# Kernel optimization log

Measured on AMD Instinct MI355X. Metric: run time of the kernel, lower is better.

## Reference

```python
import jax, jax.numpy as jnp
import numpy as np

B, S, D, EXP = 2, 2048, 128, 16
N = D * EXP  # state_dim = 2048


def setup_inputs() -> dict:
    key = jax.random.key(0)
    ks = jax.random.split(key, 11)
    s_in = 1.0 / np.sqrt(D)   # torch Linear default init bound for dim->N layers
    s_out = 1.0 / np.sqrt(N)  # for out_proj (N->dim)
    x = jax.random.normal(ks[0], (B, S, D), dtype=jnp.float32)
    W_B = jax.random.uniform(ks[1], (N, D), jnp.float32, -s_in, s_in)
    b_B = jax.random.uniform(ks[2], (N,), jnp.float32, -s_in, s_in)
    W_C = jax.random.uniform(ks[3], (N, D), jnp.float32, -s_in, s_in)
    b_C = jax.random.uniform(ks[4], (N,), jnp.float32, -s_in, s_in)
    W_dt = jax.random.uniform(ks[5], (N, D), jnp.float32, -s_in, s_in)
    b_dt = jax.random.uniform(ks[6], (N,), jnp.float32, -s_in, s_in)
    A_log = jnp.log(jax.random.uniform(ks[7], (N,), jnp.float32) * 0.5 + 0.5)
    W_out = jax.random.uniform(ks[8], (D, N), jnp.float32, -s_out, s_out)
    b_out = jax.random.uniform(ks[9], (D,), jnp.float32, -s_out, s_out)
    return {"x": x, "W_B": W_B, "b_B": b_B, "W_C": W_C, "b_C": b_C,
            "W_dt": W_dt, "b_dt": b_dt, "A_log": A_log,
            "W_out": W_out, "b_out": b_out}


def reference(x, W_B, b_B, W_C, b_C, W_dt, b_dt, A_log, W_out, b_out):
    # Featurizer projections: [B,S,D] -> [B,S,N]
    B_feat = jnp.einsum('bsd,nd->bsn', x, W_B) + b_B
    C_feat = jnp.einsum('bsd,nd->bsn', x, W_C) + b_C
    dt = jax.nn.softplus(jnp.einsum('bsd,nd->bsn', x, W_dt) + b_dt)
    A = -jnp.exp(A_log)                # [N]
    A_bar = jnp.exp(dt * A)            # [B,S,N]
    B_bar = dt * B_feat                # [B,S,N]

    # Sequential diagonal scan: h_t = A_t * h_{t-1} + B_t ; y_t = C_t * h_t
    def step(h, abc):
        a_t, b_t, c_t = abc            # each [B,N]
        h = a_t * h + b_t
        return h, c_t * h

    h0 = jnp.zeros((x.shape[0], N), dtype=x.dtype)
    xs = (jnp.swapaxes(A_bar, 0, 1),   # [S,B,N]
          jnp.swapaxes(B_bar, 0, 1),
          jnp.swapaxes(C_feat, 0, 1))
    _, ys = jax.lax.scan(step, h0, xs)  # ys: [S,B,N]
    y = jnp.swapaxes(ys, 0, 1)          # [B,S,N]
    return jnp.einsum('bsn,dn->bsd', y, W_out) + b_out
```

## Files before the change

### kernel.cpp

```cpp
#include <hip/hip_runtime.h>


#define BB 2
#define SS 2048
#define DDIM 128
#define NDIM 2048
#define TT (BB*SS)
#define NTILE (TT/16)

typedef short short8 __attribute__((ext_vector_type(8)));
typedef float floatx4 __attribute__((ext_vector_type(4)));

__device__ __forceinline__ unsigned short f2b(float f){
  unsigned u = __float_as_uint(f);
  u += 0x7FFFu + ((u >> 16) & 1u);
  return (unsigned short)(u >> 16);
}
__device__ __forceinline__ float softplus_f(float v){
  return v > 15.f ? v : __logf(1.f + __expf(v));
}
__device__ __forceinline__ void pack8(const float* __restrict__ s,
                                      unsigned short* __restrict__ d){
  floatx4 v0 = *(const floatx4*)s;
  floatx4 v1 = *(const floatx4*)(s + 4);
  short8 r;
  r[0]=(short)f2b(v0[0]); r[1]=(short)f2b(v0[1]); r[2]=(short)f2b(v0[2]); r[3]=(short)f2b(v0[3]);
  r[4]=(short)f2b(v1[0]); r[5]=(short)f2b(v1[1]); r[6]=(short)f2b(v1[2]); r[7]=(short)f2b(v1[3]);
  *(short8*)d = r;
}

__global__ void prep_kernel(const float* __restrict__ x,
                            const float* __restrict__ W_B,
                            const float* __restrict__ W_C,
                            const float* __restrict__ W_dt,
                            const float* __restrict__ A_log,
                            const float* __restrict__ W_out,
                            unsigned short* __restrict__ xp,
                            unsigned short* __restrict__ Wp3,
                            unsigned short* __restrict__ Wop,
                            float* __restrict__ Aval,
                            unsigned long long* __restrict__ Sbuf){
  const int gid = blockIdx.x * blockDim.x + threadIdx.x;
  if (gid < 32768) Sbuf[gid] = 0ull;
  if (gid < 2048) Aval[gid] = -__expf(A_log[gid]);
  if (gid < 65536){
    int g = gid, tile = g >> 8, kk = (g >> 6) & 3, lane = g & 63;
    int q = lane >> 4, m = lane & 15;
    pack8(x + (size_t)(tile*16 + m)*DDIM + kk*32 + q*8, xp + (size_t)g*8);
  }
  if (gid < 98304){
    int mat = gid >> 15, g = gid & 32767;
    const float* W = (mat == 0) ? W_B : (mat == 1 ? W_dt : W_C);
    int tile = g >> 8, kk = (g >> 6) & 3, lane = g & 63;
    int q = lane >> 4, m = lane & 15;
    pack8(W + (size_t)(tile*16 + m)*DDIM + kk*32 + q*8,
          Wp3 + (size_t)mat*262144 + (size_t)g*8);
  }
  if (gid < 32768){
    int g = gid, tile = g >> 12, kk = (g >> 6) & 63, lane = g & 63;
    int q = lane >> 4, m = lane & 15;
    pack8(W_out + (size_t)(tile*16 + m)*NDIM + kk*32 + q*8, Wop + (size_t)g*8);
  }
}

__global__ __launch_bounds__(256, 2) void projscan_kernel(
    const unsigned short* __restrict__ xp,
    const unsigned short* __restrict__ Wp3,
    const float* __restrict__ b_B,
    const float* __restrict__ b_dt,
    const float* __restrict__ b_C,
    const float* __restrict__ Aval,
    unsigned long long* __restrict__ Sbuf,
    unsigned short* __restrict__ ybp){
  __shared__ unsigned short sW[3*4096];
  __shared__ unsigned short sYT[4][16*40];
  __shared__ float sPw[4][32], sHw[4][32];
  __shared__ float sIw[4][32];
  const int tid  = threadIdx.x;
  const int lane = tid & 63;
  const int wv   = tid >> 6;
  const int m    = lane & 15;
  const int q    = lane >> 4;
  const int p    = blockIdx.y * 16 + blockIdx.x;
  const int xcd  = p & 7;
  const int slot = p >> 3;
  const int rr   = slot & 15;
  const int j    = slot >> 4;
  const int row  = xcd*16 + rr;
  const int by   = row >> 1;
  const int bx   = (row & 1)*8 + j;
  const int n0   = by*32;

  for (int i = tid; i < 1536; i += 256){
    int mat = i >> 9, rem = i & 511;
    *(short8*)(sW + mat*4096 + rem*8) =
        *(const short8*)(Wp3 + (size_t)mat*262144 + (size_t)by*4096 + rem*8);
  }
  __syncthreads();

  float bBv[2], bDv[2], bCv[2], Avv[2];
#pragma unroll
  for (int nt = 0; nt < 2; ++nt){
    const int n = n0 + nt*16 + m;
    bBv[nt] = b_B[n]; bDv[nt] = b_dt[n]; bCv[nt] = b_C[n]; Avv[nt] = Aval[n];
  }

  unsigned ypk[4][2][2], cpk[4][2][2];
  float pe_t[4][2], he_t[4][2];
  float pa_run[2] = {1.f, 1.f}, ha_run[2] = {0.f, 0.f};

#pragma unroll
  for (int i = 0; i < 4; ++i){
    const int tile = bx*16 + wv*4 + i;
    short8 xf[4];
#pragma unroll
    for (int kk = 0; kk < 4; ++kk)
      xf[kk] = *(const short8*)(xp + (size_t)tile*2048 + kk*512 + lane*8);

    floatx4 acc[3][2];
#pragma unroll
    for (int mat = 0; mat < 3; ++mat)
#pragma unroll
      for (int nt = 0; nt < 2; ++nt)
        acc[mat][nt] = (floatx4){0.f,0.f,0.f,0.f};
#pragma unroll
    for (int nt = 0; nt < 2; ++nt)
#pragma unroll
      for (int kk = 0; kk < 4; ++kk){
        short8 wB = *(const short8*)(sW +         nt*2048 + kk*512 + lane*8);
        short8 wD = *(const short8*)(sW + 4096 +  nt*2048 + kk*512 + lane*8);
        short8 wC = *(const short8*)(sW + 8192 +  nt*2048 + kk*512 + lane*8);
        acc[0][nt] = __builtin_amdgcn_mfma_f32_16x16x32_bf16(xf[kk], wB, acc[0][nt], 0, 0, 0);
        acc[1][nt] = __builtin_amdgcn_mfma_f32_16x16x32_bf16(xf[kk], wD, acc[1][nt], 0, 0, 0);
        acc[2][nt] = __builtin_amdgcn_mfma_f32_16x16x32_bf16(xf[kk], wC, acc[2][nt], 0, 0, 0);
      }

#pragma unroll
    for (int nt = 0; nt < 2; ++nt){
      float Ar[4], Br[4], Cc[4];
#pragma unroll
      for (int r = 0; r < 4; ++r){
        float dtv = softplus_f(acc[1][nt][r] + bDv[nt]);
        Ar[r] = __expf(dtv * Avv[nt]);
        Br[r] = dtv * (acc[0][nt][r] + bBv[nt]);
        Cc[r] = acc[2][nt][r] + bCv[nt];
      }
      float P = Ar[0], H = Br[0];
#pragma unroll
      for (int r = 1; r < 4; ++r){ H = Ar[r]*H + Br[r]; P *= Ar[r]; }
      float pp = __shfl(P, (lane - 16) & 63, 64);
      float hh = __shfl(H, (lane - 16) & 63, 64);
      if (q >= 1){ H = P*hh + H; P *= pp; }
      pp = __shfl(P, (lane - 32) & 63, 64);
      hh = __shfl(H, (lane - 32) & 63, 64);
      if (q >= 2){ H = P*hh + H; P *= pp; }
      float pe = __shfl(P, (lane - 16) & 63, 64);
      float he = __shfl(H, (lane - 16) & 63, 64);
      if (q == 0){ pe = 1.f; he = 0.f; }
      float pb = __shfl(P, m + 48, 64);
      float hb = __shfl(H, m + 48, 64);

      float h = he, pa = pe;
      unsigned short yr[4], cr[4];
#pragma unroll
      for (int r = 0; r < 4; ++r){
        h = Ar[r]*h + Br[r];
        pa *= Ar[r];
        yr[r] = f2b(Cc[r]*h);
        cr[r] = f2b(Cc[r]*pa);
      }
      ypk[i][nt][0] = (unsigned)yr[0] | ((unsigned)yr[1] << 16);
      ypk[i][nt][1] = (unsigned)yr[2] | ((unsigned)yr[3] << 16);
      cpk[i][nt][0] = (unsigned)cr[0] | ((unsigned)cr[1] << 16);
      cpk[i][nt][1] = (unsigned)cr[2] | ((unsigned)cr[3] << 16);

      pe_t[i][nt] = pa_run[nt];
      he_t[i][nt] = ha_run[nt];
      ha_run[nt] = pb*ha_run[nt] + hb;
      pa_run[nt] *= pb;
    }
  }
  if (q == 0){
#pragma unroll
    for (int nt = 0; nt < 2; ++nt){
      sPw[wv][nt*16 + m] = pa_run[nt];
      sHw[wv][nt*16 + m] = ha_run[nt];
    }
  }
  __syncthreads();

  if (tid < 32){
    float Pw[4], Hw[4];
#pragma unroll
    for (int w2 = 0; w2 < 4; ++w2){ Pw[w2] = sPw[w2][tid]; Hw[w2] = sHw[w2][tid]; }
    float pb = 1.f, hb = 0.f;
#pragma unroll
    for (int w2 = 0; w2 < 4; ++w2){ hb = Pw[w2]*hb + Hw[w2]; pb *= Pw[w2]; }
    float pbc = fmaxf(pb, 1e-30f);
    __hip_atomic_store(Sbuf + (size_t)(by*16 + bx)*32 + tid,
        ((unsigned long long)__float_as_uint(pbc) << 32) |
         (unsigned long long)__float_as_uint(hb),
        __ATOMIC_RELAXED, __HIP_MEMORY_SCOPE_AGENT);
    float S = 0.f;
    const int cnt = bx & 7;
    if (cnt){
      const int j0 = bx & ~7;
      unsigned long long v0=0,v1=0,v2=0,v3=0,v4=0,v5=0,v6=0;
      unsigned got = 0;
      const unsigned all = (1u << cnt) - 1u;
      const unsigned long long* base = Sbuf + (size_t)(by*16 + j0)*32 + tid;
      for (;;){
#define LOOKBACK(J, V)                                                          \
        if (J < cnt && !(got & (1u << J))){                                     \
          unsigned long long a = __hip_atomic_load(base + (size_t)J*32,         \
              __ATOMIC_RELAXED, __HIP_MEMORY_SCOPE_AGENT);                      \
          if ((unsigned)(a >> 32) != 0u){ V = a; got |= 1u << J; }              \
        }
        LOOKBACK(0, v0) LOOKBACK(1, v1) LOOKBACK(2, v2) LOOKBACK(3, v3)
        LOOKBACK(4, v4) LOOKBACK(5, v5) LOOKBACK(6, v6)
#undef LOOKBACK
        if (got == all) break;
        __builtin_amdgcn_s_sleep(1);
      }
#define COMPOSE(J, V)                                                           \
      if (J < cnt) S = __uint_as_float((unsigned)(V >> 32))*S +                 \
                       __uint_as_float((unsigned)V);
      COMPOSE(0, v0) COMPOSE(1, v1) COMPOSE(2, v2) COMPOSE(3, v3)
      COMPOSE(4, v4) COMPOSE(5, v5) COMPOSE(6, v6)
#undef COMPOSE
    }
    float s = S;
#pragma unroll
    for (int w2 = 0; w2 < 4; ++w2){
      sIw[w2][tid] = s;
      s = Pw[w2]*s + Hw[w2];
    }
  }
  __syncthreads();

  float iw[2];
#pragma unroll
  for (int nt = 0; nt < 2; ++nt) iw[nt] = sIw[wv][nt*16 + m];
#pragma unroll
  for (int i = 0; i < 4; ++i){
    const int tile = bx*16 + wv*4 + i;
#pragma unroll
    for (int nt = 0; nt < 2; ++nt){
      float it = pe_t[i][nt]*iw[nt] + he_t[i][nt];
#pragma unroll
      for (int j2 = 0; j2 < 2; ++j2){
        unsigned yp = ypk[i][nt][j2], cp = cpk[i][nt][j2];
        float y0 = __uint_as_float(yp << 16);
        float y1 = __uint_as_float(yp & 0xffff0000u);
        float c0 = __uint_as_float(cp << 16);
        float c1 = __uint_as_float(cp & 0xffff0000u);
        sYT[wv][(q*4 + j2*2 + 0)*40 + nt*16 + m] = f2b(y0 + c0*it);
        sYT[wv][(q*4 + j2*2 + 1)*40 + nt*16 + m] = f2b(y1 + c1*it);
      }
    }
    short8 yv = *(const short8*)&sYT[wv][m*40 + q*8];
    *(short8*)(ybp + (size_t)tile*32768 + (size_t)by*512 + (size_t)lane*8) = yv;
  }
}

__global__ void outproj_kernel(const unsigned short* __restrict__ ybp,
                               const unsigned short* __restrict__ Wop,
                               const float* __restrict__ b_out,
                               float* __restrict__ out){
  __shared__ float red[4*2048];
  const int tid  = threadIdx.x;
  const int lane = tid & 63;
  const int wv   = tid >> 6;
  const int m    = lane & 15;
  const int q    = lane >> 4;
  const int tile = blockIdx.x;

  floatx4 acc[8];
#pragma unroll
  for (int dt = 0; dt < 8; ++dt) acc[dt] = (floatx4){0.f,0.f,0.f,0.f};

  const unsigned short* aP = ybp + (size_t)tile*32768 + lane*8;
  const unsigned short* bP = Wop + (size_t)lane*8;
#pragma unroll 4
  for (int kk = wv*16; kk < wv*16 + 16; ++kk){
    short8 af = *(const short8*)(aP + (size_t)kk*512);
#pragma unroll
    for (int dt = 0; dt < 8; ++dt){
      short8 bf = *(const short8*)(bP + (size_t)dt*32768 + (size_t)kk*512);
      acc[dt] = __builtin_amdgcn_mfma_f32_16x16x32_bf16(af, bf, acc[dt], 0, 0, 0);
    }
  }
#pragma unroll
  for (int dt = 0; dt < 8; ++dt)
#pragma unroll
    for (int r = 0; r < 4; ++r)
      red[wv*2048 + (q*4 + r)*128 + dt*16 + m] = acc[dt][r];
  __syncthreads();
#pragma unroll
  for (int i = 0; i < 8; ++i){
    int idx = i*256 + tid;
    float s = red[idx] + red[2048 + idx] + red[4096 + idx] + red[6144 + idx];
    int tl = idx >> 7, d = idx & 127;
    out[(size_t)(tile*16 + tl)*DDIM + d] = s + b_out[d];
  }
}

extern "C" void kernel_launch(void* const* d_in, const int* in_sizes, int n_in,
                              void* d_out, int out_size, void* d_ws, size_t ws_size,
                              hipStream_t stream) {
  const float* x     = (const float*)d_in[0];
  const float* W_B   = (const float*)d_in[1];
  const float* b_B   = (const float*)d_in[2];
  const float* W_C   = (const float*)d_in[3];
  const float* b_C   = (const float*)d_in[4];
  const float* W_dt  = (const float*)d_in[5];
  const float* b_dt  = (const float*)d_in[6];
  const float* A_log = (const float*)d_in[7];
  const float* W_out = (const float*)d_in[8];
  const float* b_out = (const float*)d_in[9];
  float* out = (float*)d_out;

  char* w = (char*)d_ws;
  unsigned short* xp    = (unsigned short*)(w + 0x0000000);
  unsigned short* Wp3   = (unsigned short*)(w + 0x0100000);
  unsigned short* Wop   = (unsigned short*)(w + 0x0280000);
  float*          Aval  = (float*)         (w + 0x0300000);
  unsigned short* ybp   = (unsigned short*)(w + 0x0310000);
  unsigned long long* Sbuf = (unsigned long long*)(w + 0x1310000);

  prep_kernel<<<384, 256, 0, stream>>>(
      x, W_B, W_C, W_dt, A_log, W_out, xp, Wp3, Wop, Aval, Sbuf);

  projscan_kernel<<<dim3(16, 64), 256, 0, stream>>>(
      xp, Wp3, b_B, b_dt, b_C, Aval, Sbuf, ybp);

  outproj_kernel<<<NTILE, 256, 0, stream>>>(ybp, Wop, b_out, out);
}
```

Measured before the change: 115.5 us.

## Prefetch next x tile, use packed bf16 convert, alias LDS, back off lookback spin

The projection-scan kernel now double-buffers the x fragments, loading the next tile's inputs while the current tile's MFMAs run. Manual bf16 rounding and packing is replaced by the hardware v_cvt_pk_bf16_f32 instruction. The per-wave transpose buffer now reuses the weight LDS region after the MFMAs finish, which lowers LDS use, and the lookback spin uses an escalating sleep. Risks are higher register pressure from the double buffer, possible rounding differences from the hardware convert, and a race if any wave still reads sW when another wave writes sYT, since no barrier separates the two.

After: 115.3 us, median of 2. Within noise of the previous version (-0.2%).

```diff
diff --git a/kernel.cpp b/kernel.cpp
--- a/kernel.cpp
+++ b/kernel.cpp
@@ -15,6 +15,11 @@
   unsigned u = __float_as_uint(f);
   u += 0x7FFFu + ((u >> 16) & 1u);
   return (unsigned short)(u >> 16);
+}
+__device__ __forceinline__ unsigned cvt_pk_bf16(float lo, float hi){
+  unsigned r;
+  asm("v_cvt_pk_bf16_f32 %0, %1, %2" : "=v"(r) : "v"(lo), "v"(hi));
+  return r;
 }
 __device__ __forceinline__ float softplus_f(float v){
   return v > 15.f ? v : __logf(1.f + __expf(v));
@@ -73,7 +78,6 @@
     unsigned long long* __restrict__ Sbuf,
     unsigned short* __restrict__ ybp){
   __shared__ unsigned short sW[3*4096];
-  __shared__ unsigned short sYT[4][16*40];
   __shared__ float sPw[4][32], sHw[4][32];
   __shared__ float sIw[4][32];
   const int tid  = threadIdx.x;
@@ -90,6 +94,7 @@
   const int by   = row >> 1;
   const int bx   = (row & 1)*8 + j;
   const int n0   = by*32;
+  unsigned short* sYT = sW + wv*640;
 
   for (int i = tid; i < 1536; i += 256){
     int mat = i >> 9, rem = i & 511;
@@ -109,14 +114,17 @@
   float pe_t[4][2], he_t[4][2];
   float pa_run[2] = {1.f, 1.f}, ha_run[2] = {0.f, 0.f};
 
+  short8 xf[2][4];
+  {
+    const int t0 = bx*16 + wv*4;
+#pragma unroll
+    for (int kk = 0; kk < 4; ++kk)
+      xf[0][kk] = *(const short8*)(xp + (size_t)t0*2048 + kk*512 + lane*8);
+  }
+
 #pragma unroll
   for (int i = 0; i < 4; ++i){
-    const int tile = bx*16 + wv*4 + i;
-    short8 xf[4];
-#pragma unroll
-    for (int kk = 0; kk < 4; ++kk)
-      xf[kk] = *(const short8*)(xp + (size_t)tile*2048 + kk*512 + lane*8);
-
+    const int cur = i & 1;
     floatx4 acc[3][2];
 #pragma unroll
     for (int mat = 0; mat < 3; ++mat)
@@ -130,10 +138,16 @@
         short8 wB = *(const short8*)(sW +         nt*2048 + kk*512 + lane*8);
         short8 wD = *(const short8*)(sW + 4096 +  nt*2048 + kk*512 + lane*8);
         short8 wC = *(const short8*)(sW + 8192 +  nt*2048 + kk*512 + lane*8);
-        acc[0][nt] = __builtin_amdgcn_mfma_f32_16x16x32_bf16(xf[kk], wB, acc[0][nt], 0, 0, 0);
-        acc[1][nt] = __builtin_amdgcn_mfma_f32_16x16x32_bf16(xf[kk], wD, acc[1][nt], 0, 0, 0);
-        acc[2][nt] = __builtin_amdgcn_mfma_f32_16x16x32_bf16(xf[kk], wC, acc[2][nt], 0, 0, 0);
-      }
+        acc[0][nt] = __builtin_amdgcn_mfma_f32_16x16x32_bf16(xf[cur][kk], wB, acc[0][nt], 0, 0, 0);
+        acc[1][nt] = __builtin_amdgcn_mfma_f32_16x16x32_bf16(xf[cur][kk], wD, acc[1][nt], 0, 0, 0);
+        acc[2][nt] = __builtin_amdgcn_mfma_f32_16x16x32_bf16(xf[cur][kk], wC, acc[2][nt], 0, 0, 0);
+      }
+    if (i < 3){
+      const int t1 = bx*16 + wv*4 + i + 1;
+#pragma unroll
+      for (int kk = 0; kk < 4; ++kk)
+        xf[cur^1][kk] = *(const short8*)(xp + (size_t)t1*2048 + kk*512 + lane*8);
+    }
 
 #pragma unroll
     for (int nt = 0; nt < 2; ++nt){
@@ -161,18 +175,18 @@
       float hb = __shfl(H, m + 48, 64);
 
       float h = he, pa = pe;
-      unsigned short yr[4], cr[4];
+      float ys[4], cs[4];
 #pragma unroll
       for (int r = 0; r < 4; ++r){
         h = Ar[r]*h + Br[r];
         pa *= Ar[r];
-        yr[r] = f2b(Cc[r]*h);
-        cr[r] = f2b(Cc[r]*pa);
-      }
-      ypk[i][nt][0] = (unsigned)yr[0] | ((unsigned)yr[1] << 16);
-      ypk[i][nt][1] = (unsigned)yr[2] | ((unsigned)yr[3] << 16);
-      cpk[i][nt][0] = (unsigned)cr[0] | ((unsigned)cr[1] << 16);
-      cpk[i][nt][1] = (unsigned)cr[2] | ((unsigned)cr[3] << 16);
+        ys[r] = Cc[r]*h;
+        cs[r] = Cc[r]*pa;
+      }
+      ypk[i][nt][0] = cvt_pk_bf16(ys[0], ys[1]);
+      ypk[i][nt][1] = cvt_pk_bf16(ys[2], ys[3]);
+      cpk[i][nt][0] = cvt_pk_bf16(cs[0], cs[1]);
+      cpk[i][nt][1] = cvt_pk_bf16(cs[2], cs[3]);
 
       pe_t[i][nt] = pa_run[nt];
       he_t[i][nt] = ha_run[nt];
@@ -207,6 +221,7 @@
       const int j0 = bx & ~7;
       unsigned long long v0=0,v1=0,v2=0,v3=0,v4=0,v5=0,v6=0;
       unsigned got = 0;
+      int spin = 0;
       const unsigned all = (1u << cnt) - 1u;
       const unsigned long long* base = Sbuf + (size_t)(by*16 + j0)*32 + tid;
       for (;;){
@@ -220,7 +235,10 @@
         LOOKBACK(4, v4) LOOKBACK(5, v5) LOOKBACK(6, v6)
 #undef LOOKBACK
         if (got == all) break;
-        __builtin_amdgcn_s_sleep(1);
+        if (spin < 4)       __builtin_amdgcn_s_sleep(2);
+        else if (spin < 8)  __builtin_amdgcn_s_sleep(8);
+        else                __builtin_amdgcn_s_sleep(32);
+        ++spin;
       }
 #define COMPOSE(J, V)                                                           \
       if (J < cnt) S = __uint_as_float((unsigned)(V >> 32))*S +                 \
@@ -254,11 +272,11 @@
         float y1 = __uint_as_float(yp & 0xffff0000u);
         float c0 = __uint_as_float(cp << 16);
         float c1 = __uint_as_float(cp & 0xffff0000u);
-        sYT[wv][(q*4 + j2*2 + 0)*40 + nt*16 + m] = f2b(y0 + c0*it);
-        sYT[wv][(q*4 + j2*2 + 1)*40 + nt*16 + m] = f2b(y1 + c1*it);
-      }
-    }
-    short8 yv = *(const short8*)&sYT[wv][m*40 + q*8];
+        sYT[(q*4 + j2*2 + 0)*40 + nt*16 + m] = f2b(y0 + c0*it);
+        sYT[(q*4 + j2*2 + 1)*40 + nt*16 + m] = f2b(y1 + c1*it);
+      }
+    }
+    short8 yv = *(const short8*)&sYT[m*40 + q*8];
     *(short8*)(ybp + (size_t)tile*32768 + (size_t)by*512 + (size_t)lane*8) = yv;
   }
 }
```
